# Optimization experiments

Hardware: AMD Instinct MI355X
Metric: run time of the kernel (lower is better)

Reference implementation:

```python
import jax, jax.numpy as jnp
import numpy as np
import math

B, N, D, H = 2, 2048, 512, 8
DH = D // H
HID = int(D * 16 / 3)  # 2730, SwiGLU hidden; chunks into 1365+1365
EPS = 1e-5


def _get_slopes(n):
    # n=8 is a power of two
    start = 2.0 ** (-2.0 ** (-(math.log2(n) - 3)))
    return np.array([start * (start ** i) for i in range(n)], dtype=np.float32)

_SLOPES = jnp.asarray(_get_slopes(H))  # [H]


def _ln(x, w, b):
    m = jnp.mean(x, axis=-1, keepdims=True)
    v = jnp.mean((x - m) ** 2, axis=-1, keepdims=True)
    return (x - m) * jax.lax.rsqrt(v + EPS) * w + b


def setup_inputs() -> dict:
    key = jax.random.key(0)
    ks = jax.random.split(key, 20)
    p = lambda k, s: jax.random.normal(k, s, jnp.float32) * 0.02
    return {
        "x": jax.random.normal(ks[0], (B, N, D), jnp.float32),
        "coords": jax.random.uniform(ks[1], (B, N, 2), jnp.float32) * 100.0,
        "q_w": p(ks[2], (D, D)), "q_b": jnp.zeros((D,), jnp.float32),
        "k_w": p(ks[3], (D, D)), "k_b": jnp.zeros((D,), jnp.float32),
        "v_w": p(ks[4], (D, D)), "v_b": jnp.zeros((D,), jnp.float32),
        "o_w": p(ks[5], (D, D)), "o_b": jnp.zeros((D,), jnp.float32),
        "gamma1": jnp.ones((D,), jnp.float32),
        "ln1_w": jnp.ones((D,), jnp.float32), "ln1_b": jnp.zeros((D,), jnp.float32),
        "fc1_w": p(ks[6], (HID, D)), "fc1_b": jnp.zeros((HID,), jnp.float32),
        "fc2_w": p(ks[7], (D, HID // 2)), "fc2_b": jnp.zeros((D,), jnp.float32),
        "gamma2": jnp.ones((D,), jnp.float32),
        "ln2_w": jnp.ones((D,), jnp.float32), "ln2_b": jnp.zeros((D,), jnp.float32),
    }


def reference(x, coords, q_w, q_b, k_w, k_b, v_w, v_b, o_w, o_b, gamma1,
              ln1_w, ln1_b, fc1_w, fc1_b, fc2_w, fc2_b, gamma2, ln2_w, ln2_b):
    # ---- residual1: distance-ALiBi attention (eval mode: x + gamma1*attn(norm(x)))
    xn = _ln(x, ln1_w, ln1_b)
    q = (xn @ q_w.T + q_b).reshape(B, N, H, DH).transpose(0, 2, 1, 3)  # [b,h,n,dh]
    k = (xn @ k_w.T + k_b).reshape(B, N, H, DH).transpose(0, 2, 1, 3)
    v = (xn @ v_w.T + v_b).reshape(B, N, H, DH).transpose(0, 2, 1, 3)
    # pairwise Euclidean distance of tile coords -> [b,n,n]
    diff = coords[:, :, None, :] - coords[:, None, :, :]
    dist = jnp.sqrt(jnp.sum(diff * diff, axis=-1))
    attn_bias = -_SLOPES[None, :, None, None] * dist[:, None, :, :]  # [b,h,n,n]
    scale = 1.0 / math.sqrt(DH)
    scores = jnp.einsum('bhqd,bhkd->bhqk', q, k) * scale + attn_bias
    attn = jax.nn.softmax(scores, axis=-1)
    ctx = jnp.einsum('bhqk,bhkd->bhqd', attn, v)
    ctx = ctx.transpose(0, 2, 1, 3).reshape(B, N, D)
    attn_out = ctx @ o_w.T + o_b
    x = x + gamma1 * attn_out
    # ---- residual2: SwiGLU-style MLP (eval mode: x + gamma2*mlp(norm(x)))
    xn2 = _ln(x, ln2_w, ln2_b)
    hpre = xn2 @ fc1_w.T + fc1_b  # [b,n,HID]
    h1, h2 = jnp.split(hpre, 2, axis=-1)
    mlp_out = (jax.nn.silu(h1) * h2) @ fc2_w.T + fc2_b
    return x + gamma2 * mlp_out
```

## Files before the change

kernel.cpp:

```cpp
#include <hip/hip_runtime.h>
#include <math.h>

#define Bdim  2
#define Nseq  2048
#define Dmod  512
#define Hn    8
#define DHd   64
#define HID   2730
#define HHALF 1365
#define HC    1408
#define NPACK 2816
#define ROWS  4096
#define NSPLIT 2
#define KT_PER (Nseq / 64 / NSPLIT)

typedef __bf16 bf16x8 __attribute__((ext_vector_type(8)));
typedef __bf16 bf16x4 __attribute__((ext_vector_type(4)));
typedef float  f32x4  __attribute__((ext_vector_type(4)));

__device__ __forceinline__ void glds16(const __bf16* g, __bf16* l) {
    __builtin_amdgcn_global_load_lds(
        (const __attribute__((address_space(1))) void*)g,
        (__attribute__((address_space(3))) void*)l, 16, 0, 0);
}

__device__ __forceinline__ void ln_body(
    int row, int tid, const float* __restrict__ x, const float* __restrict__ w,
    const float* __restrict__ b, __bf16* __restrict__ out)
{
    const float* xr = x + (size_t)row * Dmod;
    float2 v = *(const float2*)(xr + tid * 2);
    float s  = v.x + v.y;
    float sq = v.x * v.x + v.y * v.y;
#pragma unroll
    for (int m = 1; m < 64; m <<= 1) {
        s  += __shfl_xor(s, m, 64);
        sq += __shfl_xor(sq, m, 64);
    }
    __shared__ float ss[4], ssq[4];
    const int wv = tid >> 6;
    if ((tid & 63) == 0) { ss[wv] = s; ssq[wv] = sq; }
    __syncthreads();
    s  = ss[0] + ss[1] + ss[2] + ss[3];
    sq = ssq[0] + ssq[1] + ssq[2] + ssq[3];
    const float mean = s * (1.0f / Dmod);
    const float var  = sq * (1.0f / Dmod) - mean * mean;
    const float rstd = rsqrtf(var + 1e-5f);
    float2 wv2 = *(const float2*)(w + tid * 2);
    float2 bv2 = *(const float2*)(b + tid * 2);
    __bf16* orow = out + (size_t)row * Dmod + tid * 2;
    orow[0] = (__bf16)((v.x - mean) * rstd * wv2.x + bv2.x);
    orow[1] = (__bf16)((v.y - mean) * rstd * wv2.y + bv2.y);
}

#define SEG0 (1536*512)
#define SEG1 (512*512)
#define SEG2 (NPACK*512)
#define SEG3 (512*HC)
#define CONV_BLOCKS ((SEG0 + SEG1 + SEG2 + SEG3) / 256)
__global__ __launch_bounds__(256) void convert_ln(
    const float* __restrict__ q_w, const float* __restrict__ k_w,
    const float* __restrict__ v_w, const float* __restrict__ o_w,
    const float* __restrict__ fc1_w, const float* __restrict__ fc2_w,
    __bf16* __restrict__ wqkv, __bf16* __restrict__ wo,
    __bf16* __restrict__ wfc1p, __bf16* __restrict__ wfc2p,
    const float* __restrict__ x, const float* __restrict__ ln1w,
    const float* __restrict__ ln1b, __bf16* __restrict__ xn)
{
    if (blockIdx.x >= CONV_BLOCKS) {
        ln_body(blockIdx.x - CONV_BLOCKS, threadIdx.x, x, ln1w, ln1b, xn);
        return;
    }
    int idx = blockIdx.x * 256 + threadIdx.x;
    if (idx < SEG0) {
        int n = idx >> 9, k = idx & 511;
        float v = (n < 512) ? q_w[n * 512 + k]
                : (n < 1024) ? k_w[(n - 512) * 512 + k]
                : v_w[(n - 1024) * 512 + k];
        wqkv[idx] = (__bf16)v;
        return;
    }
    idx -= SEG0;
    if (idx < SEG1) { wo[idx] = (__bf16)o_w[idx]; return; }
    idx -= SEG1;
    if (idx < SEG2) {
        int n = idx >> 9, k = idx & 511;
        int j = n >> 5, u = n & 31;
        int base = j * 16 + (u & 15);
        float v = 0.0f;
        if (base < HHALF) {
            int hidx = base + ((u & 16) ? HHALF : 0);
            v = fc1_w[(size_t)hidx * 512 + k];
        }
        wfc1p[idx] = (__bf16)v;
        return;
    }
    idx -= SEG2;
    if (idx < SEG3) {
        int n = idx / HC, k = idx - n * HC;
        float v = (k < HHALF) ? fc2_w[(size_t)n * HHALF + k] : 0.0f;
        wfc2p[idx] = (__bf16)v;
    }
}

__global__ __launch_bounds__(256) void ln_kernel(
    const float* __restrict__ x, const float* __restrict__ w,
    const float* __restrict__ b, __bf16* __restrict__ out)
{
    ln_body(blockIdx.x, threadIdx.x, x, w, b, out);
}

__global__ __launch_bounds__(512) void gemm_res(
    const __bf16* __restrict__ A, int lda,
    const __bf16* __restrict__ Bw, int ldb,
    const float* __restrict__ bias, int K,
    float* __restrict__ out_f32, int ld_out,
    const float* __restrict__ res, const float* __restrict__ g)
{
    __shared__ __bf16 smem[2 * 64 * 64];
    __bf16* As = smem;
    __bf16* Bs = smem + 64 * 64;
    const int tid  = threadIdx.x;
    const int wave = tid >> 6, lane = tid & 63;
    const int t    = lane & 15, quad = lane >> 4;
    const int kg   = wave >> 2, wv = wave & 3;
    const int m0   = blockIdx.x * 64;
    const int n0   = blockIdx.y * 64;

    const int srow = tid >> 3;
    const int gch  = ((tid & 7) ^ (srow & 7)) * 8;
    const __bf16* aptr = A  + (size_t)(m0 + srow) * lda + gch;
    const __bf16* bptr = Bw + (size_t)(n0 + srow) * ldb + gch;

    const int arow = wv * 16 + t;
    const int aoff = arow * 64 + (((kg * 4 + quad) ^ (arow & 7)) * 8);
    int boffs[4];
#pragma unroll
    for (int ct = 0; ct < 4; ++ct) {
        int brow = ct * 16 + t;
        boffs[ct] = brow * 64 + (((kg * 4 + quad) ^ (brow & 7)) * 8);
    }

    f32x4 acc[4] = {};
    for (int k0 = 0; k0 < K; k0 += 64) {
        __syncthreads();
        glds16(aptr + k0, As + tid * 8);
        glds16(bptr + k0, Bs + tid * 8);
        __syncthreads();
        bf16x8 a = *(const bf16x8*)(As + aoff);
#pragma unroll
        for (int ct = 0; ct < 4; ++ct) {
            bf16x8 b = *(const bf16x8*)(Bs + boffs[ct]);
            acc[ct] = __builtin_amdgcn_mfma_f32_16x16x32_bf16(a, b, acc[ct], 0, 0, 0);
        }
    }

    __syncthreads();
    if (kg == 1) {
        float* dst = (float*)smem + ((size_t)wv * 64 + lane) * 16;
#pragma unroll
        for (int ct = 0; ct < 4; ++ct) *(f32x4*)(dst + ct * 4) = acc[ct];
    }
    __syncthreads();
    if (kg == 0) {
        const float* src = (const float*)smem + ((size_t)wv * 64 + lane) * 16;
        const int row_base = m0 + wv * 16 + quad * 4;
#pragma unroll
        for (int ct = 0; ct < 4; ++ct) {
            f32x4 other = *(const f32x4*)(src + ct * 4);
            const int col = n0 + ct * 16 + t;
            const float bb = bias[col];
#pragma unroll
            for (int r = 0; r < 4; ++r) {
                const int row = row_base + r;
                out_f32[(size_t)row * ld_out + col] =
                    res[(size_t)row * ld_out + col] +
                    g[col] * (acc[ct][r] + other[r] + bb);
            }
        }
    }
}

#define LDT 136
__global__ __launch_bounds__(256) void qkv_gemm128(
    const __bf16* __restrict__ A, const __bf16* __restrict__ W,
    const float* __restrict__ qb_, const float* __restrict__ kb_,
    const float* __restrict__ vb_,
    __bf16* __restrict__ qk, __bf16* __restrict__ vtg)
{
    __shared__ __bf16 smem[64 * LDT];
    __bf16* As = smem;
    __bf16* Bs = smem + 4096;
    const int tid  = threadIdx.x;
    const int wave = tid >> 6, lane = tid & 63;
    const int t    = lane & 15, quad = lane >> 4;
    const int m0   = blockIdx.x * 128, n0 = blockIdx.y * 128;
    const int mr   = (wave & 1) * 64,  nr = (wave >> 1) * 64;
    const int ra0 = tid >> 2,          ca0 = (tid & 3) * 8;
    const int ra1 = (tid + 256) >> 2,  ca1 = (tid & 3) * 8;

    f32x4 acc[4][4] = {};

    for (int k0 = 0; k0 < Dmod; k0 += 32) {
        __syncthreads();
        glds16(A + (size_t)(m0 + ra0) * Dmod + k0 + ca0, As + tid * 8);
        glds16(A + (size_t)(m0 + ra1) * Dmod + k0 + ca1, As + (tid + 256) * 8);
        glds16(W + (size_t)(n0 + ra0) * Dmod + k0 + ca0, Bs + tid * 8);
        glds16(W + (size_t)(n0 + ra1) * Dmod + k0 + ca1, Bs + (tid + 256) * 8);
        __syncthreads();
        bf16x8 af[4], bfr[4];
#pragma unroll
        for (int mi = 0; mi < 4; ++mi)
            af[mi] = *(const bf16x8*)(As + (mr + mi * 16 + t) * 32 + quad * 8);
#pragma unroll
        for (int ni = 0; ni < 4; ++ni)
            bfr[ni] = *(const bf16x8*)(Bs + (nr + ni * 16 + t) * 32 + quad * 8);
#pragma unroll
        for (int mi = 0; mi < 4; ++mi)
#pragma unroll
            for (int ni = 0; ni < 4; ++ni)
                acc[mi][ni] = __builtin_amdgcn_mfma_f32_16x16x32_bf16(af[mi], bfr[ni], acc[mi][ni], 0, 0, 0);
    }

    const int y = blockIdx.y;
    if (y < 8) {
#pragma unroll
        for (int mi = 0; mi < 4; ++mi) {
            const int row_base = m0 + mr + mi * 16 + quad * 4;
#pragma unroll
            for (int ni = 0; ni < 4; ++ni) {
                const int col = n0 + nr + ni * 16 + t;
                const float bb = (col < 512) ? qb_[col] : kb_[col - 512];
#pragma unroll
                for (int r = 0; r < 4; ++r)
                    qk[(size_t)(row_base + r) * 1024 + col] = (__bf16)(acc[mi][ni][r] + bb);
            }
        }
    } else {
        const int tok0 = m0 & 2047;
        const int bI   = m0 >> 11;
#pragma unroll
        for (int half = 0; half < 2; ++half) {
            __syncthreads();
            if ((wave >> 1) == half) {
#pragma unroll
                for (int ni = 0; ni < 4; ++ni) {
                    const int dh = ni * 16 + t;
                    const float bb = vb_[(y - 8) * 128 + half * 64 + dh];
#pragma unroll
                    for (int mi = 0; mi < 4; ++mi) {
                        const int n = mr + mi * 16 + quad * 4;
                        bf16x4 pk;
#pragma unroll
                        for (int r = 0; r < 4; ++r) pk[r] = (__bf16)(acc[mi][ni][r] + bb);
                        *(bf16x4*)(smem + dh * LDT + n) = pk;
                    }
                }
            }
            __syncthreads();
            const int hh = (y - 8) * 2 + half;
            const size_t rowbase = (size_t)(bI * 8 + hh) * 64;
#pragma unroll
            for (int j = 0; j < 4; ++j) {
                int chunk = tid + j * 256;
                int dr = chunk >> 4, cc = (chunk & 15) * 8;
                bf16x8 vv = *(const bf16x8*)(smem + dr * LDT + cc);
                *(bf16x8*)(vtg + (rowbase + dr) * Nseq + tok0 + cc) = vv;
            }
        }
    }
}

__global__ __launch_bounds__(256) void fc1_gemm128(
    const __bf16* __restrict__ A, const __bf16* __restrict__ W,
    const float* __restrict__ fc1_b_, __bf16* __restrict__ out)
{
    __shared__ __bf16 As[128 * 32];
    __shared__ __bf16 Bs[128 * 32];
    const int tid  = threadIdx.x;
    const int wave = tid >> 6, lane = tid & 63;
    const int t    = lane & 15, quad = lane >> 4;
    const int m0   = blockIdx.x * 128, n0 = blockIdx.y * 128;
    const int mr   = (wave & 1) * 64,  nr = (wave >> 1) * 64;
    const int ra0 = tid >> 2,          ca0 = (tid & 3) * 8;
    const int ra1 = (tid + 256) >> 2,  ca1 = (tid & 3) * 8;

    f32x4 acc[4][4] = {};

    for (int k0 = 0; k0 < Dmod; k0 += 32) {
        __syncthreads();
        glds16(A + (size_t)(m0 + ra0) * Dmod + k0 + ca0, As + tid * 8);
        glds16(A + (size_t)(m0 + ra1) * Dmod + k0 + ca1, As + (tid + 256) * 8);
        glds16(W + (size_t)(n0 + ra0) * Dmod + k0 + ca0, Bs + tid * 8);
        glds16(W + (size_t)(n0 + ra1) * Dmod + k0 + ca1, Bs + (tid + 256) * 8);
        __syncthreads();
        bf16x8 af[4], bfr[4];
#pragma unroll
        for (int mi = 0; mi < 4; ++mi)
            af[mi] = *(const bf16x8*)(As + (mr + mi * 16 + t) * 32 + quad * 8);
#pragma unroll
        for (int ni = 0; ni < 4; ++ni)
            bfr[ni] = *(const bf16x8*)(Bs + (nr + ni * 16 + t) * 32 + quad * 8);
#pragma unroll
        for (int mi = 0; mi < 4; ++mi)
#pragma unroll
            for (int ni = 0; ni < 4; ++ni)
                acc[mi][ni] = __builtin_amdgcn_mfma_f32_16x16x32_bf16(af[mi], bfr[ni], acc[mi][ni], 0, 0, 0);
    }

#pragma unroll
    for (int mi = 0; mi < 4; ++mi) {
        const int row_base = m0 + mr + mi * 16 + quad * 4;
#pragma unroll
        for (int gI = 0; gI < 2; ++gI) {
            const int base = n0 + nr + gI * 32;
            const int hb = (base >> 5) * 16 + t;
            const bool valid = hb < HHALF;
            const float b1 = valid ? fc1_b_[hb] : 0.0f;
            const float b2 = valid ? fc1_b_[HHALF + hb] : 0.0f;
#pragma unroll
            for (int r = 0; r < 4; ++r) {
                float a = acc[mi][2 * gI][r] + b1;
                float c = acc[mi][2 * gI + 1][r] + b2;
                float sw = a / (1.0f + __expf(-a)) * c;
                out[(size_t)(row_base + r) * HC + hb] = (__bf16)sw;
            }
        }
    }
}

__global__ __launch_bounds__(256) void attn_kernel(
    const __bf16* __restrict__ qk, const __bf16* __restrict__ vt,
    const float* __restrict__ coords,
    __bf16* __restrict__ op, float* __restrict__ lp)
{
    constexpr int LD = 72;
    __shared__ __bf16 Ks[64][LD];
    __shared__ __bf16 Vt[64][LD];
    __shared__ __bf16 Ps[64][LD];
    __shared__ float2 kco[64];

    const int qt = blockIdx.x, h = blockIdx.y;
    const int s = blockIdx.z >> 1, b = blockIdx.z & 1;
    const int bh = b * Hn + h;
    const int tid = threadIdx.x;
    const int wave = tid >> 6, lane = tid & 63;
    const int t = lane & 15, quad = lane >> 4;
    const float c1 = 0.125f * 1.44269504f;
    const float d1 = exp2f(-(float)(h + 1)) * 1.44269504f;
    const int kt0 = s * KT_PER, kt1 = kt0 + KT_PER;

    const int qrow = qt * 64 + wave * 16 + t;
    const size_t qbase = (size_t)(b * Nseq + qrow) * 1024 + h * DHd;
    bf16x8 bq0 = *(const bf16x8*)(qk + qbase + quad * 8);
    bf16x8 bq1 = *(const bf16x8*)(qk + qbase + 32 + quad * 8);
    float2 qc = *(const float2*)(coords + (size_t)(b * Nseq + qrow) * 2);
    const float qx = qc.x, qy = qc.y;

    const int sr = tid >> 3, scc = (tid & 7) * 8;
    const __bf16* kbase = qk + (size_t)(b * Nseq) * 1024 + 512 + h * DHd;
    const __bf16* vbase = vt + (size_t)(bh * 64) * Nseq;

    bf16x8 kreg0, kreg1, vreg0, vreg1;
    float2 kcreg = {0.f, 0.f};
    {
        const int kn0 = kt0 * 64;
        kreg0 = *(const bf16x8*)(kbase + (size_t)(kn0 + sr) * 1024 + scc);
        kreg1 = *(const bf16x8*)(kbase + (size_t)(kn0 + sr + 32) * 1024 + scc);
        vreg0 = *(const bf16x8*)(vbase + (size_t)sr * Nseq + kn0 + scc);
        vreg1 = *(const bf16x8*)(vbase + (size_t)(sr + 32) * Nseq + kn0 + scc);
        if (tid < 64) kcreg = *(const float2*)(coords + (size_t)(b * Nseq + kn0 + tid) * 2);
    }

    f32x4 o[4] = {};
    float lrun = 0.0f;

    for (int kt = kt0; kt < kt1; ++kt) {
        __syncthreads();
        *(bf16x8*)(&Ks[sr][scc])      = kreg0;
        *(bf16x8*)(&Ks[sr + 32][scc]) = kreg1;
        *(bf16x8*)(&Vt[sr][scc])      = vreg0;
        *(bf16x8*)(&Vt[sr + 32][scc]) = vreg1;
        if (tid < 64) kco[tid] = kcreg;
        __syncthreads();
        if (kt + 1 < kt1) {
            const int kn = (kt + 1) * 64;
            kreg0 = *(const bf16x8*)(kbase + (size_t)(kn + sr) * 1024 + scc);
            kreg1 = *(const bf16x8*)(kbase + (size_t)(kn + sr + 32) * 1024 + scc);
            vreg0 = *(const bf16x8*)(vbase + (size_t)sr * Nseq + kn + scc);
            vreg1 = *(const bf16x8*)(vbase + (size_t)(sr + 32) * Nseq + kn + scc);
            if (tid < 64) kcreg = *(const float2*)(coords + (size_t)(b * Nseq + kn + tid) * 2);
        }

        f32x4 sA[4];
#pragma unroll
        for (int am = 0; am < 4; ++am) {
            bf16x8 a0 = *(const bf16x8*)(&Ks[am * 16 + t][quad * 8]);
            bf16x8 a1 = *(const bf16x8*)(&Ks[am * 16 + t][32 + quad * 8]);
            f32x4 z = {};
            z = __builtin_amdgcn_mfma_f32_16x16x32_bf16(a0, bq0, z, 0, 0, 0);
            sA[am] = __builtin_amdgcn_mfma_f32_16x16x32_bf16(a1, bq1, z, 0, 0, 0);
        }

        float p[4][4];
#pragma unroll
        for (int am = 0; am < 4; ++am)
#pragma unroll
            for (int r = 0; r < 4; ++r) {
                float2 kc = kco[am * 16 + quad * 4 + r];
                float dx = qx - kc.x, dy = qy - kc.y;
                float dist = __builtin_amdgcn_sqrtf(dx * dx + dy * dy);
                float e = __builtin_amdgcn_exp2f(sA[am][r] * c1 - d1 * dist);
                p[am][r] = e;
                lrun += e;
            }

#pragma unroll
        for (int am = 0; am < 4; ++am) {
            bf16x4 pk;
#pragma unroll
            for (int r = 0; r < 4; ++r) pk[r] = (__bf16)p[am][r];
            *(bf16x4*)(&Ps[wave * 16 + t][am * 16 + quad * 4]) = pk;
        }

        bf16x8 ap0 = *(const bf16x8*)(&Ps[wave * 16 + t][quad * 8]);
        bf16x8 ap1 = *(const bf16x8*)(&Ps[wave * 16 + t][32 + quad * 8]);
#pragma unroll
        for (int ct = 0; ct < 4; ++ct) {
            bf16x8 bv0 = *(const bf16x8*)(&Vt[ct * 16 + t][quad * 8]);
            bf16x8 bv1 = *(const bf16x8*)(&Vt[ct * 16 + t][32 + quad * 8]);
            o[ct] = __builtin_amdgcn_mfma_f32_16x16x32_bf16(ap0, bv0, o[ct], 0, 0, 0);
            o[ct] = __builtin_amdgcn_mfma_f32_16x16x32_bf16(ap1, bv1, o[ct], 0, 0, 0);
        }
    }

    lrun += __shfl_xor(lrun, 16, 64);
    lrun += __shfl_xor(lrun, 32, 64);
    if (quad == 0)
        lp[(((size_t)s * Bdim + b) * Hn + h) * Nseq + qt * 64 + wave * 16 + t] = lrun;

    const int orow_base = qt * 64 + wave * 16 + quad * 4;
#pragma unroll
    for (int ct = 0; ct < 4; ++ct)
#pragma unroll
        for (int r = 0; r < 4; ++r) {
            size_t row = (size_t)s * ROWS + b * Nseq + orow_base + r;
            op[row * Dmod + h * DHd + ct * 16 + t] = (__bf16)o[ct][r];
        }
}

__global__ __launch_bounds__(256) void merge_kernel(
    const __bf16* __restrict__ op, const float* __restrict__ lp,
    __bf16* __restrict__ ctx)
{
    int idx = blockIdx.x * 256 + threadIdx.x;
    int row = idx >> 7, c4 = (idx & 127) * 4;
    int h = c4 >> 6;
    int b = row >> 11, n = row & 2047;
    float l = 0.0f;
#pragma unroll
    for (int s = 0; s < NSPLIT; ++s)
        l += lp[(((size_t)s * Bdim + b) * Hn + h) * Nseq + n];
    float rl = __builtin_amdgcn_rcpf(l);
    float oa[4] = {0.f, 0.f, 0.f, 0.f};
#pragma unroll
    for (int s = 0; s < NSPLIT; ++s) {
        bf16x4 ov = *(const bf16x4*)(op + ((size_t)s * ROWS + row) * Dmod + c4);
#pragma unroll
        for (int j = 0; j < 4; ++j) oa[j] += (float)ov[j];
    }
    bf16x4 r;
#pragma unroll
    for (int j = 0; j < 4; ++j) r[j] = (__bf16)(oa[j] * rl);
    *(bf16x4*)(ctx + (size_t)row * Dmod + c4) = r;
}

extern "C" void kernel_launch(void* const* d_in, const int* in_sizes, int n_in,
                              void* d_out, int out_size, void* d_ws, size_t ws_size,
                              hipStream_t stream)
{
    (void)in_sizes; (void)n_in; (void)out_size; (void)ws_size;
    const float* x      = (const float*)d_in[0];
    const float* coords = (const float*)d_in[1];
    const float* q_w    = (const float*)d_in[2];
    const float* q_b    = (const float*)d_in[3];
    const float* k_w    = (const float*)d_in[4];
    const float* k_b    = (const float*)d_in[5];
    const float* v_w    = (const float*)d_in[6];
    const float* v_b    = (const float*)d_in[7];
    const float* o_w    = (const float*)d_in[8];
    const float* o_b    = (const float*)d_in[9];
    const float* gamma1 = (const float*)d_in[10];
    const float* ln1_w  = (const float*)d_in[11];
    const float* ln1_b  = (const float*)d_in[12];
    const float* fc1_w  = (const float*)d_in[13];
    const float* fc1_b  = (const float*)d_in[14];
    const float* fc2_w  = (const float*)d_in[15];
    const float* fc2_b  = (const float*)d_in[16];
    const float* gamma2 = (const float*)d_in[17];
    const float* ln2_w  = (const float*)d_in[18];
    const float* ln2_b  = (const float*)d_in[19];

    size_t off = 0;
    auto alloc = [&](size_t bytes) {
        void* p = (char*)d_ws + off;
        off += (bytes + 255) & ~(size_t)255;
        return p;
    };
    __bf16* wqkv  = (__bf16*)alloc((size_t)1536 * 512 * 2);
    __bf16* wo    = (__bf16*)alloc((size_t)512 * 512 * 2);
    __bf16* wfc1p = (__bf16*)alloc((size_t)NPACK * 512 * 2);
    __bf16* wfc2p = (__bf16*)alloc((size_t)512 * HC * 2);
    __bf16* xn    = (__bf16*)alloc((size_t)ROWS * Dmod * 2);
    __bf16* xn2   = (__bf16*)alloc((size_t)ROWS * Dmod * 2);
    __bf16* qkb   = (__bf16*)alloc((size_t)ROWS * 1024 * 2);
    __bf16* vtg   = (__bf16*)alloc((size_t)Bdim * Hn * DHd * Nseq * 2);
    __bf16* ctxb  = (__bf16*)alloc((size_t)ROWS * Dmod * 2);
    float*  x1    = (float*)alloc((size_t)ROWS * Dmod * 4);
    __bf16* hcomb = (__bf16*)alloc((size_t)ROWS * HC * 2);
    __bf16* opb   = (__bf16*)alloc((size_t)NSPLIT * ROWS * Dmod * 2);
    float*  lpb   = (float*)alloc((size_t)NSPLIT * Bdim * Hn * Nseq * 4);

    convert_ln<<<CONV_BLOCKS + ROWS, 256, 0, stream>>>(
        q_w, k_w, v_w, o_w, fc1_w, fc2_w, wqkv, wo, wfc1p, wfc2p,
        x, ln1_w, ln1_b, xn);

    qkv_gemm128<<<dim3(ROWS / 128, 12), 256, 0, stream>>>(xn, wqkv, q_b, k_b, v_b, qkb, vtg);

    attn_kernel<<<dim3(Nseq / 64, Hn, Bdim * NSPLIT), 256, 0, stream>>>(
        qkb, vtg, coords, opb, lpb);
    merge_kernel<<<(ROWS * 128 + 255) / 256, 256, 0, stream>>>(opb, lpb, ctxb);

    gemm_res<<<dim3(ROWS / 64, Dmod / 64), 512, 0, stream>>>(
        ctxb, Dmod, wo, Dmod, o_b, Dmod, x1, Dmod, x, gamma1);

    ln_kernel<<<ROWS, 256, 0, stream>>>(x1, ln2_w, ln2_b, xn2);

    fc1_gemm128<<<dim3(ROWS / 128, NPACK / 128), 256, 0, stream>>>(xn2, wfc1p, fc1_b, hcomb);

    gemm_res<<<dim3(ROWS / 64, Dmod / 64), 512, 0, stream>>>(
        hcomb, HC, wfc2p, HC, fc2_b, HC, (float*)d_out, Dmod, x1, gamma2);
}
```

Baseline: 218.4 us.

## Widen GEMM K-tiles to 64 with swizzled LDS, drop split-K, and split attention four ways

The residual GEMM drops its intra-block split-K over two wave groups. It now runs 256 threads, each covering the full 64-wide K tile, with two MFMA halves per step. This removes the LDS reduction and its extra barriers. The QKV and fc1 128x128 GEMMs go from 32-wide to 64-wide K tiles with XOR-swizzled LDS, halving the number of barrier-separated iterations at double the LDS footprint. Attention's KV split rises from 2 to 4 to expose more parallelism, at the cost of more partial-output traffic and merge work.

```diff
diff --git a/kernel.cpp b/kernel.cpp
--- a/kernel.cpp
+++ b/kernel.cpp
@@ -11,8 +11,7 @@
 #define HC    1408
 #define NPACK 2816
 #define ROWS  4096
-#define NSPLIT 2
-#define KT_PER (Nseq / 64 / NSPLIT)
+#define NSPLIT 4
 
 typedef __bf16 bf16x8 __attribute__((ext_vector_type(8)));
 typedef __bf16 bf16x4 __attribute__((ext_vector_type(4)));
@@ -110,7 +109,7 @@
     ln_body(blockIdx.x, threadIdx.x, x, w, b, out);
 }
 
-__global__ __launch_bounds__(512) void gemm_res(
+__global__ __launch_bounds__(256) void gemm_res(
     const __bf16* __restrict__ A, int lda,
     const __bf16* __restrict__ Bw, int ldb,
     const float* __restrict__ bias, int K,
@@ -123,63 +122,96 @@
     const int tid  = threadIdx.x;
     const int wave = tid >> 6, lane = tid & 63;
     const int t    = lane & 15, quad = lane >> 4;
-    const int kg   = wave >> 2, wv = wave & 3;
     const int m0   = blockIdx.x * 64;
     const int n0   = blockIdx.y * 64;
 
-    const int srow = tid >> 3;
-    const int gch  = ((tid & 7) ^ (srow & 7)) * 8;
-    const __bf16* aptr = A  + (size_t)(m0 + srow) * lda + gch;
-    const __bf16* bptr = Bw + (size_t)(n0 + srow) * ldb + gch;
-
-    const int arow = wv * 16 + t;
-    const int aoff = arow * 64 + (((kg * 4 + quad) ^ (arow & 7)) * 8);
-    int boffs[4];
-#pragma unroll
-    for (int ct = 0; ct < 4; ++ct) {
-        int brow = ct * 16 + t;
-        boffs[ct] = brow * 64 + (((kg * 4 + quad) ^ (brow & 7)) * 8);
-    }
-
+    const int r0 = tid >> 3,           p0 = tid & 7;
+    const int r1 = (tid + 256) >> 3,   p1 = tid & 7;
+    const int g0 = (p0 ^ (r0 & 7)) * 8;
+    const int g1 = (p1 ^ (r1 & 7)) * 8;
+    const __bf16* a0p = A  + (size_t)(m0 + r0) * lda + g0;
+    const __bf16* a1p = A  + (size_t)(m0 + r1) * lda + g1;
+    const __bf16* b0p = Bw + (size_t)(n0 + r0) * ldb + g0;
+    const __bf16* b1p = Bw + (size_t)(n0 + r1) * ldb + g1;
+
+    const int sw = t & 7;
     f32x4 acc[4] = {};
+
     for (int k0 = 0; k0 < K; k0 += 64) {
         __syncthreads();
-        glds16(aptr + k0, As + tid * 8);
-        glds16(bptr + k0, Bs + tid * 8);
+        glds16(a0p + k0, As + tid * 8);
+        glds16(a1p + k0, As + (tid + 256) * 8);
+        glds16(b0p + k0, Bs + tid * 8);
+        glds16(b1p + k0, Bs + (tid + 256) * 8);
         __syncthreads();
-        bf16x8 a = *(const bf16x8*)(As + aoff);
-#pragma unroll
-        for (int ct = 0; ct < 4; ++ct) {
-            bf16x8 b = *(const bf16x8*)(Bs + boffs[ct]);
-            acc[ct] = __builtin_amdgcn_mfma_f32_16x16x32_bf16(a, b, acc[ct], 0, 0, 0);
-        }
-    }
-
-    __syncthreads();
-    if (kg == 1) {
-        float* dst = (float*)smem + ((size_t)wv * 64 + lane) * 16;
-#pragma unroll
-        for (int ct = 0; ct < 4; ++ct) *(f32x4*)(dst + ct * 4) = acc[ct];
-    }
-    __syncthreads();
-    if (kg == 0) {
-        const float* src = (const float*)smem + ((size_t)wv * 64 + lane) * 16;
-        const int row_base = m0 + wv * 16 + quad * 4;
-#pragma unroll
-        for (int ct = 0; ct < 4; ++ct) {
-            f32x4 other = *(const f32x4*)(src + ct * 4);
-            const int col = n0 + ct * 16 + t;
-            const float bb = bias[col];
-#pragma unroll
-            for (int r = 0; r < 4; ++r) {
-                const int row = row_base + r;
-                out_f32[(size_t)row * ld_out + col] =
-                    res[(size_t)row * ld_out + col] +
-                    g[col] * (acc[ct][r] + other[r] + bb);
+#pragma unroll
+        for (int half = 0; half < 2; ++half) {
+            const int co = ((half * 4 + quad) ^ sw) * 8;
+            bf16x8 a = *(const bf16x8*)(As + (wave * 16 + t) * 64 + co);
+#pragma unroll
+            for (int ct = 0; ct < 4; ++ct) {
+                bf16x8 b = *(const bf16x8*)(Bs + (ct * 16 + t) * 64 + co);
+                acc[ct] = __builtin_amdgcn_mfma_f32_16x16x32_bf16(a, b, acc[ct], 0, 0, 0);
             }
         }
     }
-}
+
+    const int row_base = m0 + wave * 16 + quad * 4;
+#pragma unroll
+    for (int ct = 0; ct < 4; ++ct) {
+        const int col = n0 + ct * 16 + t;
+        const float bb = bias[col];
+#pragma unroll
+        for (int r = 0; r < 4; ++r) {
+            const int row = row_base + r;
+            out_f32[(size_t)row * ld_out + col] =
+                res[(size_t)row * ld_out + col] + g[col] * (acc[ct][r] + bb);
+        }
+    }
+}
+
+#define QKV_KLOOP(A_, W_, KTOT)                                                   \
+    for (int k0 = 0; k0 < (KTOT); k0 += 64) {                                     \
+        __syncthreads();                                                          \
+        glds16(A_ + (size_t)(m0 + ar0) * Dmod + k0 + ag0, As + tid * 8);          \
+        glds16(A_ + (size_t)(m0 + ar1) * Dmod + k0 + ag1, As + (tid + 256) * 8);  \
+        glds16(A_ + (size_t)(m0 + ar2) * Dmod + k0 + ag2, As + (tid + 512) * 8);  \
+        glds16(A_ + (size_t)(m0 + ar3) * Dmod + k0 + ag3, As + (tid + 768) * 8);  \
+        glds16(W_ + (size_t)(n0 + ar0) * Dmod + k0 + ag0, Bs + tid * 8);          \
+        glds16(W_ + (size_t)(n0 + ar1) * Dmod + k0 + ag1, Bs + (tid + 256) * 8);  \
+        glds16(W_ + (size_t)(n0 + ar2) * Dmod + k0 + ag2, Bs + (tid + 512) * 8);  \
+        glds16(W_ + (size_t)(n0 + ar3) * Dmod + k0 + ag3, Bs + (tid + 768) * 8);  \
+        __syncthreads();                                                          \
+        _Pragma("unroll")                                                         \
+        for (int half = 0; half < 2; ++half) {                                    \
+            const int co = ((half * 4 + quad) ^ sw) * 8;                          \
+            bf16x8 af[4], bfr[4];                                                 \
+            _Pragma("unroll")                                                     \
+            for (int mi = 0; mi < 4; ++mi)                                        \
+                af[mi] = *(const bf16x8*)(As + (mr + mi * 16 + t) * 64 + co);     \
+            _Pragma("unroll")                                                     \
+            for (int ni = 0; ni < 4; ++ni)                                        \
+                bfr[ni] = *(const bf16x8*)(Bs + (nr + ni * 16 + t) * 64 + co);    \
+            _Pragma("unroll")                                                     \
+            for (int mi = 0; mi < 4; ++mi)                                        \
+                _Pragma("unroll")                                                 \
+                for (int ni = 0; ni < 4; ++ni)                                    \
+                    acc[mi][ni] = __builtin_amdgcn_mfma_f32_16x16x32_bf16(        \
+                        af[mi], bfr[ni], acc[mi][ni], 0, 0, 0);                   \
+        }                                                                         \
+    }
+
+#define GEMM128_SETUP                                                   \
+    const int tid  = threadIdx.x;                                       \
+    const int wave = tid >> 6, lane = tid & 63;                         \
+    const int t    = lane & 15, quad = lane >> 4;                       \
+    const int m0   = blockIdx.x * 128, n0 = blockIdx.y * 128;           \
+    const int mr   = (wave & 1) * 64,  nr = (wave >> 1) * 64;           \
+    const int ar0 = tid >> 3,          ag0 = ((tid & 7) ^ (ar0 & 7)) * 8;  \
+    const int ar1 = (tid + 256) >> 3,  ag1 = ((tid & 7) ^ (ar1 & 7)) * 8;  \
+    const int ar2 = (tid + 512) >> 3,  ag2 = ((tid & 7) ^ (ar2 & 7)) * 8;  \
+    const int ar3 = (tid + 768) >> 3,  ag3 = ((tid & 7) ^ (ar3 & 7)) * 8;  \
+    const int sw  = t & 7;
 
 #define LDT 136
 __global__ __launch_bounds__(256) void qkv_gemm128(
@@ -188,39 +220,12 @@
     const float* __restrict__ vb_,
     __bf16* __restrict__ qk, __bf16* __restrict__ vtg)
 {
-    __shared__ __bf16 smem[64 * LDT];
+    __shared__ __bf16 smem[2 * 128 * 64];
     __bf16* As = smem;
-    __bf16* Bs = smem + 4096;
-    const int tid  = threadIdx.x;
-    const int wave = tid >> 6, lane = tid & 63;
-    const int t    = lane & 15, quad = lane >> 4;
-    const int m0   = blockIdx.x * 128, n0 = blockIdx.y * 128;
-    const int mr   = (wave & 1) * 64,  nr = (wave >> 1) * 64;
-    const int ra0 = tid >> 2,          ca0 = (tid & 3) * 8;
-    const int ra1 = (tid + 256) >> 2,  ca1 = (tid & 3) * 8;
-
+    __bf16* Bs = smem + 8192;
+    GEMM128_SETUP
     f32x4 acc[4][4] = {};
-
-    for (int k0 = 0; k0 < Dmod; k0 += 32) {
-        __syncthreads();
-        glds16(A + (size_t)(m0 + ra0) * Dmod + k0 + ca0, As + tid * 8);
-        glds16(A + (size_t)(m0 + ra1) * Dmod + k0 + ca1, As + (tid + 256) * 8);
-        glds16(W + (size_t)(n0 + ra0) * Dmod + k0 + ca0, Bs + tid * 8);
-        glds16(W + (size_t)(n0 + ra1) * Dmod + k0 + ca1, Bs + (tid + 256) * 8);
-        __syncthreads();
-        bf16x8 af[4], bfr[4];
-#pragma unroll
-        for (int mi = 0; mi < 4; ++mi)
-            af[mi] = *(const bf16x8*)(As + (mr + mi * 16 + t) * 32 + quad * 8);
-#pragma unroll
-        for (int ni = 0; ni < 4; ++ni)
-            bfr[ni] = *(const bf16x8*)(Bs + (nr + ni * 16 + t) * 32 + quad * 8);
-#pragma unroll
-        for (int mi = 0; mi < 4; ++mi)
-#pragma unroll
-            for (int ni = 0; ni < 4; ++ni)
-                acc[mi][ni] = __builtin_amdgcn_mfma_f32_16x16x32_bf16(af[mi], bfr[ni], acc[mi][ni], 0, 0, 0);
-    }
+    QKV_KLOOP(A, W, Dmod)
 
     const int y = blockIdx.y;
     if (y < 8) {
@@ -275,38 +280,12 @@
     const __bf16* __restrict__ A, const __bf16* __restrict__ W,
     const float* __restrict__ fc1_b_, __bf16* __restrict__ out)
 {
-    __shared__ __bf16 As[128 * 32];
-    __shared__ __bf16 Bs[128 * 32];
-    const int tid  = threadIdx.x;
-    const int wave = tid >> 6, lane = tid & 63;
-    const int t    = lane & 15, quad = lane >> 4;
-    const int m0   = blockIdx.x * 128, n0 = blockIdx.y * 128;
-    const int mr   = (wave & 1) * 64,  nr = (wave >> 1) * 64;
-    const int ra0 = tid >> 2,          ca0 = (tid & 3) * 8;
-    const int ra1 = (tid + 256) >> 2,  ca1 = (tid & 3) * 8;
-
+    __shared__ __bf16 smem[2 * 128 * 64];
+    __bf16* As = smem;
+    __bf16* Bs = smem + 8192;
+    GEMM128_SETUP
     f32x4 acc[4][4] = {};
-
-    for (int k0 = 0; k0 < Dmod; k0 += 32) {
-        __syncthreads();
-        glds16(A + (size_t)(m0 + ra0) * Dmod + k0 + ca0, As + tid * 8);
-        glds16(A + (size_t)(m0 + ra1) * Dmod + k0 + ca1, As + (tid + 256) * 8);
-        glds16(W + (size_t)(n0 + ra0) * Dmod + k0 + ca0, Bs + tid * 8);
-        glds16(W + (size_t)(n0 + ra1) * Dmod + k0 + ca1, Bs + (tid + 256) * 8);
-        __syncthreads();
-        bf16x8 af[4], bfr[4];
-#pragma unroll
-        for (int mi = 0; mi < 4; ++mi)
-            af[mi] = *(const bf16x8*)(As + (mr + mi * 16 + t) * 32 + quad * 8);
-#pragma unroll
-        for (int ni = 0; ni < 4; ++ni)
-            bfr[ni] = *(const bf16x8*)(Bs + (nr + ni * 16 + t) * 32 + quad * 8);
-#pragma unroll
-        for (int mi = 0; mi < 4; ++mi)
-#pragma unroll
-            for (int ni = 0; ni < 4; ++ni)
-                acc[mi][ni] = __builtin_amdgcn_mfma_f32_16x16x32_bf16(af[mi], bfr[ni], acc[mi][ni], 0, 0, 0);
-    }
+    QKV_KLOOP(A, W, Dmod)
 
 #pragma unroll
     for (int mi = 0; mi < 4; ++mi) {
@@ -322,8 +301,8 @@
             for (int r = 0; r < 4; ++r) {
                 float a = acc[mi][2 * gI][r] + b1;
                 float c = acc[mi][2 * gI + 1][r] + b2;
-                float sw = a / (1.0f + __expf(-a)) * c;
-                out[(size_t)(row_base + r) * HC + hb] = (__bf16)sw;
+                float sw2 = a / (1.0f + __expf(-a)) * c;
+                out[(size_t)(row_base + r) * HC + hb] = (__bf16)sw2;
             }
         }
     }
@@ -332,7 +311,7 @@
 __global__ __launch_bounds__(256) void attn_kernel(
     const __bf16* __restrict__ qk, const __bf16* __restrict__ vt,
     const float* __restrict__ coords,
-    __bf16* __restrict__ op, float* __restrict__ lp)
+    __bf16* __restrict__ op, float* __restrict__ lp, int ktper)
 {
     constexpr int LD = 72;
     __shared__ __bf16 Ks[64][LD];
@@ -348,7 +327,6 @@
     const int t = lane & 15, quad = lane >> 4;
     const float c1 = 0.125f * 1.44269504f;
     const float d1 = exp2f(-(float)(h + 1)) * 1.44269504f;
-    const int kt0 = s * KT_PER, kt1 = kt0 + KT_PER;
 
     const int qrow = qt * 64 + wave * 16 + t;
     const size_t qbase = (size_t)(b * Nseq + qrow) * 1024 + h * DHd;
@@ -363,19 +341,17 @@
 
     bf16x8 kreg0, kreg1, vreg0, vreg1;
     float2 kcreg = {0.f, 0.f};
-    {
-        const int kn0 = kt0 * 64;
-        kreg0 = *(const bf16x8*)(kbase + (size_t)(kn0 + sr) * 1024 + scc);
-        kreg1 = *(const bf16x8*)(kbase + (size_t)(kn0 + sr + 32) * 1024 + scc);
-        vreg0 = *(const bf16x8*)(vbase + (size_t)sr * Nseq + kn0 + scc);
-        vreg1 = *(const bf16x8*)(vbase + (size_t)(sr + 32) * Nseq + kn0 + scc);
-        if (tid < 64) kcreg = *(const float2*)(coords + (size_t)(b * Nseq + kn0 + tid) * 2);
-    }
+    int kn = s * ktper * 64;
+    kreg0 = *(const bf16x8*)(kbase + (size_t)(kn + sr) * 1024 + scc);
+    kreg1 = *(const bf16x8*)(kbase + (size_t)(kn + sr + 32) * 1024 + scc);
+    vreg0 = *(const bf16x8*)(vbase + (size_t)sr * Nseq + kn + scc);
+    vreg1 = *(const bf16x8*)(vbase + (size_t)(sr + 32) * Nseq + kn + scc);
+    if (tid < 64) kcreg = *(const float2*)(coords + (size_t)(b * Nseq + kn + tid) * 2);
 
     f32x4 o[4] = {};
     float lrun = 0.0f;
 
-    for (int kt = kt0; kt < kt1; ++kt) {
+    for (int it = 0; it < ktper; ++it) {
         __syncthreads();
         *(bf16x8*)(&Ks[sr][scc])      = kreg0;
         *(bf16x8*)(&Ks[sr + 32][scc]) = kreg1;
@@ -383,13 +359,13 @@
         *(bf16x8*)(&Vt[sr + 32][scc]) = vreg1;
         if (tid < 64) kco[tid] = kcreg;
         __syncthreads();
-        if (kt + 1 < kt1) {
-            const int kn = (kt + 1) * 64;
-            kreg0 = *(const bf16x8*)(kbase + (size_t)(kn + sr) * 1024 + scc);
-            kreg1 = *(const bf16x8*)(kbase + (size_t)(kn + sr + 32) * 1024 + scc);
-            vreg0 = *(const bf16x8*)(vbase + (size_t)sr * Nseq + kn + scc);
-            vreg1 = *(const bf16x8*)(vbase + (size_t)(sr + 32) * Nseq + kn + scc);
-            if (tid < 64) kcreg = *(const float2*)(coords + (size_t)(b * Nseq + kn + tid) * 2);
+        if (it + 1 < ktper) {
+            const int k2 = kn + 64;
+            kreg0 = *(const bf16x8*)(kbase + (size_t)(k2 + sr) * 1024 + scc);
+            kreg1 = *(const bf16x8*)(kbase + (size_t)(k2 + sr + 32) * 1024 + scc);
+            vreg0 = *(const bf16x8*)(vbase + (size_t)sr * Nseq + k2 + scc);
+            vreg1 = *(const bf16x8*)(vbase + (size_t)(sr + 32) * Nseq + k2 + scc);
+            if (tid < 64) kcreg = *(const float2*)(coords + (size_t)(b * Nseq + k2 + tid) * 2);
         }
 
         f32x4 sA[4];
@@ -432,6 +408,7 @@
             o[ct] = __builtin_amdgcn_mfma_f32_16x16x32_bf16(ap0, bv0, o[ct], 0, 0, 0);
             o[ct] = __builtin_amdgcn_mfma_f32_16x16x32_bf16(ap1, bv1, o[ct], 0, 0, 0);
         }
+        kn += 64;
     }
 
     lrun += __shfl_xor(lrun, 16, 64);
@@ -528,16 +505,16 @@
     qkv_gemm128<<<dim3(ROWS / 128, 12), 256, 0, stream>>>(xn, wqkv, q_b, k_b, v_b, qkb, vtg);
 
     attn_kernel<<<dim3(Nseq / 64, Hn, Bdim * NSPLIT), 256, 0, stream>>>(
-        qkb, vtg, coords, opb, lpb);
+        qkb, vtg, coords, opb, lpb, Nseq / 64 / NSPLIT);
     merge_kernel<<<(ROWS * 128 + 255) / 256, 256, 0, stream>>>(opb, lpb, ctxb);
 
-    gemm_res<<<dim3(ROWS / 64, Dmod / 64), 512, 0, stream>>>(
+    gemm_res<<<dim3(ROWS / 64, Dmod / 64), 256, 0, stream>>>(
         ctxb, Dmod, wo, Dmod, o_b, Dmod, x1, Dmod, x, gamma1);
 
     ln_kernel<<<ROWS, 256, 0, stream>>>(x1, ln2_w, ln2_b, xn2);
 
     fc1_gemm128<<<dim3(ROWS / 128, NPACK / 128), 256, 0, stream>>>(xn2, wfc1p, fc1_b, hcomb);
 
-    gemm_res<<<dim3(ROWS / 64, Dmod / 64), 512, 0, stream>>>(
+    gemm_res<<<dim3(ROWS / 64, Dmod / 64), 256, 0, stream>>>(
         hcomb, HC, wfc2p, HC, fc2_b, HC, (float*)d_out, Dmod, x1, gamma2);
 }
```

After: 225.0 us. 1.03x slower.

## Precompute pairwise distance matrix in fp16 and stream it into attention

Applied to the files above, without the earlier changes.

Adds a pass inside the convert/LN kernel that computes the full B×N×N Euclidean distance matrix in fp16 and writes it to workspace. The attention kernel then loads distance tiles through registers into an XOR-swizzled LDS buffer instead of computing sqrt from coordinates per score, and the split length becomes a runtime argument. This removes per-score sqrt and coordinate LDS reads from the attention inner loop, but adds about 16 MB of global writes plus a redundant re-read of each batch's distances for every head (8 heads), and fp16 distances lose precision.

```diff
diff --git a/kernel.cpp b/kernel.cpp
--- a/kernel.cpp
+++ b/kernel.cpp
@@ -12,11 +12,12 @@
 #define NPACK 2816
 #define ROWS  4096
 #define NSPLIT 2
-#define KT_PER (Nseq / 64 / NSPLIT)
-
-typedef __bf16 bf16x8 __attribute__((ext_vector_type(8)));
-typedef __bf16 bf16x4 __attribute__((ext_vector_type(4)));
-typedef float  f32x4  __attribute__((ext_vector_type(4)));
+
+typedef __bf16    bf16x8 __attribute__((ext_vector_type(8)));
+typedef __bf16    bf16x4 __attribute__((ext_vector_type(4)));
+typedef float     f32x4  __attribute__((ext_vector_type(4)));
+typedef _Float16  f16x8  __attribute__((ext_vector_type(8)));
+typedef _Float16  f16x4  __attribute__((ext_vector_type(4)));
 
 __device__ __forceinline__ void glds16(const __bf16* g, __bf16* l) {
     __builtin_amdgcn_global_load_lds(
@@ -58,6 +59,7 @@
 #define SEG2 (NPACK*512)
 #define SEG3 (512*HC)
 #define CONV_BLOCKS ((SEG0 + SEG1 + SEG2 + SEG3) / 256)
+#define DIST_BLOCKS (Bdim * Nseq * Nseq / 256)
 __global__ __launch_bounds__(256) void convert_ln(
     const float* __restrict__ q_w, const float* __restrict__ k_w,
     const float* __restrict__ v_w, const float* __restrict__ o_w,
@@ -65,8 +67,20 @@
     __bf16* __restrict__ wqkv, __bf16* __restrict__ wo,
     __bf16* __restrict__ wfc1p, __bf16* __restrict__ wfc2p,
     const float* __restrict__ x, const float* __restrict__ ln1w,
-    const float* __restrict__ ln1b, __bf16* __restrict__ xn)
-{
+    const float* __restrict__ ln1b, __bf16* __restrict__ xn,
+    const float* __restrict__ coords, _Float16* __restrict__ db)
+{
+    if (blockIdx.x >= CONV_BLOCKS + ROWS) {
+        int idx = (blockIdx.x - CONV_BLOCKS - ROWS) * 256 + threadIdx.x;
+        int b = idx >> 22;
+        int rem = idx & ((1 << 22) - 1);
+        int q = rem >> 11, k = rem & 2047;
+        float2 cq = *(const float2*)(coords + ((size_t)b * Nseq + q) * 2);
+        float2 ck = *(const float2*)(coords + ((size_t)b * Nseq + k) * 2);
+        float dx = cq.x - ck.x, dy = cq.y - ck.y;
+        db[idx] = (_Float16)__builtin_amdgcn_sqrtf(dx * dx + dy * dy);
+        return;
+    }
     if (blockIdx.x >= CONV_BLOCKS) {
         ln_body(blockIdx.x - CONV_BLOCKS, threadIdx.x, x, ln1w, ln1b, xn);
         return;
@@ -331,14 +345,14 @@
 
 __global__ __launch_bounds__(256) void attn_kernel(
     const __bf16* __restrict__ qk, const __bf16* __restrict__ vt,
-    const float* __restrict__ coords,
-    __bf16* __restrict__ op, float* __restrict__ lp)
+    const _Float16* __restrict__ db,
+    __bf16* __restrict__ op, float* __restrict__ lp, int ktper)
 {
     constexpr int LD = 72;
     __shared__ __bf16 Ks[64][LD];
     __shared__ __bf16 Vt[64][LD];
     __shared__ __bf16 Ps[64][LD];
-    __shared__ float2 kco[64];
+    __shared__ _Float16 Dds[64 * 64];
 
     const int qt = blockIdx.x, h = blockIdx.y;
     const int s = blockIdx.z >> 1, b = blockIdx.z & 1;
@@ -348,48 +362,54 @@
     const int t = lane & 15, quad = lane >> 4;
     const float c1 = 0.125f * 1.44269504f;
     const float d1 = exp2f(-(float)(h + 1)) * 1.44269504f;
-    const int kt0 = s * KT_PER, kt1 = kt0 + KT_PER;
 
     const int qrow = qt * 64 + wave * 16 + t;
     const size_t qbase = (size_t)(b * Nseq + qrow) * 1024 + h * DHd;
     bf16x8 bq0 = *(const bf16x8*)(qk + qbase + quad * 8);
     bf16x8 bq1 = *(const bf16x8*)(qk + qbase + 32 + quad * 8);
-    float2 qc = *(const float2*)(coords + (size_t)(b * Nseq + qrow) * 2);
-    const float qx = qc.x, qy = qc.y;
 
     const int sr = tid >> 3, scc = (tid & 7) * 8;
     const __bf16* kbase = qk + (size_t)(b * Nseq) * 1024 + 512 + h * DHd;
     const __bf16* vbase = vt + (size_t)(bh * 64) * Nseq;
+    const _Float16* dbase = db + ((size_t)b * Nseq + qt * 64 + sr) * Nseq
+                               + ((tid & 7) ^ (sr & 7)) * 8;
+
+    const int qv = wave * 16 + t;
+    int doff[4];
+#pragma unroll
+    for (int am = 0; am < 4; ++am)
+        doff[am] = qv * 64 + (((am * 2 + (quad >> 1)) ^ (t & 7)) * 8) + (quad & 1) * 4;
 
     bf16x8 kreg0, kreg1, vreg0, vreg1;
-    float2 kcreg = {0.f, 0.f};
-    {
-        const int kn0 = kt0 * 64;
-        kreg0 = *(const bf16x8*)(kbase + (size_t)(kn0 + sr) * 1024 + scc);
-        kreg1 = *(const bf16x8*)(kbase + (size_t)(kn0 + sr + 32) * 1024 + scc);
-        vreg0 = *(const bf16x8*)(vbase + (size_t)sr * Nseq + kn0 + scc);
-        vreg1 = *(const bf16x8*)(vbase + (size_t)(sr + 32) * Nseq + kn0 + scc);
-        if (tid < 64) kcreg = *(const float2*)(coords + (size_t)(b * Nseq + kn0 + tid) * 2);
-    }
+    f16x8 dreg0, dreg1;
+    int kn = s * ktper * 64;
+    kreg0 = *(const bf16x8*)(kbase + (size_t)(kn + sr) * 1024 + scc);
+    kreg1 = *(const bf16x8*)(kbase + (size_t)(kn + sr + 32) * 1024 + scc);
+    vreg0 = *(const bf16x8*)(vbase + (size_t)sr * Nseq + kn + scc);
+    vreg1 = *(const bf16x8*)(vbase + (size_t)(sr + 32) * Nseq + kn + scc);
+    dreg0 = *(const f16x8*)(dbase + kn);
+    dreg1 = *(const f16x8*)(dbase + (size_t)32 * Nseq + kn);
 
     f32x4 o[4] = {};
     float lrun = 0.0f;
 
-    for (int kt = kt0; kt < kt1; ++kt) {
+    for (int it = 0; it < ktper; ++it) {
         __syncthreads();
         *(bf16x8*)(&Ks[sr][scc])      = kreg0;
         *(bf16x8*)(&Ks[sr + 32][scc]) = kreg1;
         *(bf16x8*)(&Vt[sr][scc])      = vreg0;
         *(bf16x8*)(&Vt[sr + 32][scc]) = vreg1;
-        if (tid < 64) kco[tid] = kcreg;
-        __syncthreads();
-        if (kt + 1 < kt1) {
-            const int kn = (kt + 1) * 64;
-            kreg0 = *(const bf16x8*)(kbase + (size_t)(kn + sr) * 1024 + scc);
-            kreg1 = *(const bf16x8*)(kbase + (size_t)(kn + sr + 32) * 1024 + scc);
-            vreg0 = *(const bf16x8*)(vbase + (size_t)sr * Nseq + kn + scc);
-            vreg1 = *(const bf16x8*)(vbase + (size_t)(sr + 32) * Nseq + kn + scc);
-            if (tid < 64) kcreg = *(const float2*)(coords + (size_t)(b * Nseq + kn + tid) * 2);
+        *(f16x8*)(Dds + tid * 8)         = dreg0;
+        *(f16x8*)(Dds + (tid + 256) * 8) = dreg1;
+        __syncthreads();
+        if (it + 1 < ktper) {
+            const int k2 = kn + 64;
+            kreg0 = *(const bf16x8*)(kbase + (size_t)(k2 + sr) * 1024 + scc);
+            kreg1 = *(const bf16x8*)(kbase + (size_t)(k2 + sr + 32) * 1024 + scc);
+            vreg0 = *(const bf16x8*)(vbase + (size_t)sr * Nseq + k2 + scc);
+            vreg1 = *(const bf16x8*)(vbase + (size_t)(sr + 32) * Nseq + k2 + scc);
+            dreg0 = *(const f16x8*)(dbase + k2);
+            dreg1 = *(const f16x8*)(dbase + (size_t)32 * Nseq + k2);
         }
 
         f32x4 sA[4];
@@ -404,16 +424,15 @@
 
         float p[4][4];
 #pragma unroll
-        for (int am = 0; am < 4; ++am)
+        for (int am = 0; am < 4; ++am) {
+            f16x4 dv = *(const f16x4*)(Dds + doff[am]);
 #pragma unroll
             for (int r = 0; r < 4; ++r) {
-                float2 kc = kco[am * 16 + quad * 4 + r];
-                float dx = qx - kc.x, dy = qy - kc.y;
-                float dist = __builtin_amdgcn_sqrtf(dx * dx + dy * dy);
-                float e = __builtin_amdgcn_exp2f(sA[am][r] * c1 - d1 * dist);
+                float e = __builtin_amdgcn_exp2f(sA[am][r] * c1 - d1 * (float)dv[r]);
                 p[am][r] = e;
                 lrun += e;
             }
+        }
 
 #pragma unroll
         for (int am = 0; am < 4; ++am) {
@@ -432,6 +451,7 @@
             o[ct] = __builtin_amdgcn_mfma_f32_16x16x32_bf16(ap0, bv0, o[ct], 0, 0, 0);
             o[ct] = __builtin_amdgcn_mfma_f32_16x16x32_bf16(ap1, bv1, o[ct], 0, 0, 0);
         }
+        kn += 64;
     }
 
     lrun += __shfl_xor(lrun, 16, 64);
@@ -507,28 +527,29 @@
         off += (bytes + 255) & ~(size_t)255;
         return p;
     };
-    __bf16* wqkv  = (__bf16*)alloc((size_t)1536 * 512 * 2);
-    __bf16* wo    = (__bf16*)alloc((size_t)512 * 512 * 2);
-    __bf16* wfc1p = (__bf16*)alloc((size_t)NPACK * 512 * 2);
-    __bf16* wfc2p = (__bf16*)alloc((size_t)512 * HC * 2);
-    __bf16* xn    = (__bf16*)alloc((size_t)ROWS * Dmod * 2);
-    __bf16* xn2   = (__bf16*)alloc((size_t)ROWS * Dmod * 2);
-    __bf16* qkb   = (__bf16*)alloc((size_t)ROWS * 1024 * 2);
-    __bf16* vtg   = (__bf16*)alloc((size_t)Bdim * Hn * DHd * Nseq * 2);
-    __bf16* ctxb  = (__bf16*)alloc((size_t)ROWS * Dmod * 2);
-    float*  x1    = (float*)alloc((size_t)ROWS * Dmod * 4);
-    __bf16* hcomb = (__bf16*)alloc((size_t)ROWS * HC * 2);
-    __bf16* opb   = (__bf16*)alloc((size_t)NSPLIT * ROWS * Dmod * 2);
-    float*  lpb   = (float*)alloc((size_t)NSPLIT * Bdim * Hn * Nseq * 4);
-
-    convert_ln<<<CONV_BLOCKS + ROWS, 256, 0, stream>>>(
+    __bf16*   wqkv  = (__bf16*)alloc((size_t)1536 * 512 * 2);
+    __bf16*   wo    = (__bf16*)alloc((size_t)512 * 512 * 2);
+    __bf16*   wfc1p = (__bf16*)alloc((size_t)NPACK * 512 * 2);
+    __bf16*   wfc2p = (__bf16*)alloc((size_t)512 * HC * 2);
+    __bf16*   xn    = (__bf16*)alloc((size_t)ROWS * Dmod * 2);
+    __bf16*   xn2   = (__bf16*)alloc((size_t)ROWS * Dmod * 2);
+    __bf16*   qkb   = (__bf16*)alloc((size_t)ROWS * 1024 * 2);
+    __bf16*   vtg   = (__bf16*)alloc((size_t)Bdim * Hn * DHd * Nseq * 2);
+    __bf16*   ctxb  = (__bf16*)alloc((size_t)ROWS * Dmod * 2);
+    float*    x1    = (float*)alloc((size_t)ROWS * Dmod * 4);
+    __bf16*   hcomb = (__bf16*)alloc((size_t)ROWS * HC * 2);
+    __bf16*   opb   = (__bf16*)alloc((size_t)NSPLIT * ROWS * Dmod * 2);
+    float*    lpb   = (float*)alloc((size_t)NSPLIT * Bdim * Hn * Nseq * 4);
+    _Float16* distb = (_Float16*)alloc((size_t)Bdim * Nseq * Nseq * 2);
+
+    convert_ln<<<CONV_BLOCKS + ROWS + DIST_BLOCKS, 256, 0, stream>>>(
         q_w, k_w, v_w, o_w, fc1_w, fc2_w, wqkv, wo, wfc1p, wfc2p,
-        x, ln1_w, ln1_b, xn);
+        x, ln1_w, ln1_b, xn, coords, distb);
 
     qkv_gemm128<<<dim3(ROWS / 128, 12), 256, 0, stream>>>(xn, wqkv, q_b, k_b, v_b, qkb, vtg);
 
     attn_kernel<<<dim3(Nseq / 64, Hn, Bdim * NSPLIT), 256, 0, stream>>>(
-        qkb, vtg, coords, opb, lpb);
+        qkb, vtg, distb, opb, lpb, Nseq / 64 / NSPLIT);
     merge_kernel<<<(ROWS * 128 + 255) / 256, 256, 0, stream>>>(opb, lpb, ctxb);
 
     gemm_res<<<dim3(ROWS / 64, Dmod / 64), 512, 0, stream>>>(
```

Result: slower. 233.7 us (+7.0%).
